# Kernel optimization log

Hardware: AMD Instinct MI355X
Metric: run time of the kernel (lower is better)

The kernel has to match this reference:

```python
import jax, jax.numpy as jnp
import numpy as np

B, C, HH, WW = 8, 512, 32, 32
HEADS, GROUPS, EPS = 8, 32, 1e-5


def setup_inputs() -> dict:
    key = jax.random.key(0)
    k0, k1, k2 = jax.random.split(key, 3)
    x = jax.random.normal(k0, (B, C, HH, WW), jnp.float32)
    gamma = jnp.ones((C,), jnp.float32)
    beta = jnp.zeros((C,), jnp.float32)
    # 1x1 convs modeled as (out, in) matrices; fan-in scaling keeps logits sane
    w_qkv = jax.random.normal(k1, (3 * C, C), jnp.float32) * (C ** -0.5)
    b_qkv = jnp.zeros((3 * C,), jnp.float32)
    w_proj = jax.random.normal(k2, (C, C), jnp.float32) * (C ** -0.5)
    b_proj = jnp.zeros((C,), jnp.float32)
    return {"x": x, "gamma": gamma, "beta": beta, "w_qkv": w_qkv,
            "b_qkv": b_qkv, "w_proj": w_proj, "b_proj": b_proj}


def reference(x, gamma, beta, w_qkv, b_qkv, w_proj, b_proj):
    b, c, h, w = x.shape
    S = h * w
    xr = x.reshape(b, c, S)
    # GroupNorm(32, C) over (channels_in_group, spatial)
    xg = xr.reshape(b, GROUPS, c // GROUPS, S)
    mu = xg.mean(axis=(2, 3), keepdims=True)
    var = xg.var(axis=(2, 3), keepdims=True)
    xn = ((xg - mu) * jax.lax.rsqrt(var + EPS)).reshape(b, c, S)
    xn = xn * gamma[None, :, None] + beta[None, :, None]
    # qkv 1x1 conv: (B, 3C, S)
    qkv = jnp.einsum('oc,bcs->bos', w_qkv, xn) + b_qkv[None, :, None]
    D = c // HEADS
    qkv = qkv.reshape(b, 3, HEADS, D, S)  # channel layout: (three, H, D)
    q = jnp.transpose(qkv[:, 0], (0, 1, 3, 2))  # (B, H, S, D)
    k = jnp.transpose(qkv[:, 1], (0, 1, 3, 2))
    v = jnp.transpose(qkv[:, 2], (0, 1, 3, 2))
    scale = 1.0 / float(np.sqrt(np.sqrt(D)))
    logits = jnp.einsum('bhtd,bhsd->bhts', q * scale, k * scale)  # (B,H,S,S)
    logits = logits - jnp.max(logits, axis=-1, keepdims=True)
    probs = jax.nn.softmax(logits, axis=-1)  # dropout p=0 (default)
    attn = jnp.einsum('bhts,bhsd->bhtd', probs, v)  # (B,H,S,D)
    hout = jnp.transpose(attn, (0, 1, 3, 2)).reshape(b, c, S)  # (B, H*D=C, S)
    hout = jnp.einsum('oc,bcs->bos', w_proj, hout) + b_proj[None, :, None]
    return (hout + xr).reshape(b, c, h, w)
```

## Files before the change

kernel.cpp:

```cpp
#include <hip/hip_runtime.h>
#include <hip/hip_bf16.h>

typedef __hip_bfloat16 bf16;
typedef unsigned short u16;
typedef __attribute__((ext_vector_type(8))) short bf16x8;
typedef __attribute__((ext_vector_type(4))) float f32x4;
typedef __attribute__((ext_vector_type(16))) float f32x16;

static constexpr int Bn = 8;
static constexpr int C = 512;
static constexpr int S = 1024;
static constexpr int NH = 8;
static constexpr int HD = 64;
static constexpr int CPG = 16;
#define EPSV 1e-5f
#define QSCALE 0.18033688011112042f

__device__ __forceinline__ u16 f2bf(float f) {
    bf16 h = __float2bfloat16(f);
    return *reinterpret_cast<u16*>(&h);
}
__device__ __forceinline__ unsigned pack_bf2(float a, float b) {
    __hip_bfloat162 h = __float22bfloat162_rn(make_float2(a, b));
    return *reinterpret_cast<unsigned*>(&h);
}

__device__ __forceinline__ void async_copy16(const void* g, void* l) {
    __builtin_amdgcn_global_load_lds(
        (const __attribute__((address_space(1))) void*)g,
        (__attribute__((address_space(3))) void*)l, 16, 0, 0);
}

__global__ __launch_bounds__(256) void prep(const float* __restrict__ x,
                                            const float* __restrict__ wqkv,
                                            const float* __restrict__ wproj,
                                            float* __restrict__ stats,
                                            u16* __restrict__ wbf) {
    const int tid = threadIdx.x;
    if (blockIdx.x < 256) {
        const int bg = blockIdx.x;
        const size_t base = (size_t)bg * CPG * S;
        const int N = CPG * S;
        float sum = 0.f, sq = 0.f;
        for (int i = tid * 4; i < N; i += 1024) {
            float4 v = *reinterpret_cast<const float4*>(&x[base + i]);
            sum += v.x + v.y + v.z + v.w;
            sq += v.x * v.x + v.y * v.y + v.z * v.z + v.w * v.w;
        }
#pragma unroll
        for (int off = 32; off > 0; off >>= 1) {
            sum += __shfl_down(sum, off, 64);
            sq  += __shfl_down(sq,  off, 64);
        }
        __shared__ float s0[4], s1[4];
        if ((tid & 63) == 0) { s0[tid >> 6] = sum; s1[tid >> 6] = sq; }
        __syncthreads();
        if (tid == 0) {
            float a  = s0[0] + s0[1] + s0[2] + s0[3];
            float b2 = s1[0] + s1[1] + s1[2] + s1[3];
            float mu = a / (float)N;
            float var = fmaxf(b2 / (float)N - mu * mu, 0.f);
            stats[bg] = mu;
            stats[256 + bg] = rsqrtf(var + EPSV);
        }
    } else {
        int idx = (blockIdx.x - 256) * 1024 + tid * 4;
        float4 v;
        float sc = 1.f;
        if (idx < 1536 * 512) {
            v = *reinterpret_cast<const float4*>(&wqkv[idx]);
            if (idx < 512 * 512) sc = QSCALE;
        } else {
            v = *reinterpret_cast<const float4*>(&wproj[idx - 1536 * 512]);
        }
        u16 t[4] = {f2bf(v.x * sc), f2bf(v.y * sc), f2bf(v.z * sc), f2bf(v.w * sc)};
        *reinterpret_cast<uint2*>(&wbf[idx]) = *reinterpret_cast<uint2*>(t);
    }
}

__global__ __launch_bounds__(256) void gn_apply_t(const float* __restrict__ x,
                                                  const float* __restrict__ gamma,
                                                  const float* __restrict__ beta,
                                                  const float* __restrict__ stats,
                                                  u16* __restrict__ xnt) {
    const int b = blockIdx.z, c0 = blockIdx.y * 64, s0 = blockIdx.x * 64;
    const int tid = threadIdx.x;
    __shared__ u16 T[64 * 72];
    const float* xb = x + ((size_t)b * C + c0) * S;
#pragma unroll
    for (int i = 0; i < 4; ++i) {
        int ch = i * 256 + tid;
        int c = ch >> 4, seg = ch & 15;
        int cg = c0 + c;
        float mu = stats[b * 32 + (cg >> 4)];
        float rstd = stats[256 + b * 32 + (cg >> 4)];
        float ga = gamma[cg], be = beta[cg];
        float4 v = *reinterpret_cast<const float4*>(&xb[(size_t)c * S + s0 + seg * 4]);
        float vals[4] = {v.x, v.y, v.z, v.w};
#pragma unroll
        for (int j = 0; j < 4; ++j)
            T[(seg * 4 + j) * 72 + c] = f2bf((vals[j] - mu) * rstd * ga + be);
    }
    __syncthreads();
#pragma unroll
    for (int i = 0; i < 2; ++i) {
        int ch = i * 256 + tid;
        int r = ch >> 3, seg = ch & 7;
        uint4 val = *reinterpret_cast<const uint4*>(&T[r * 72 + seg * 8]);
        *reinterpret_cast<uint4*>(&xnt[(size_t)(b * S + s0 + r) * C + c0 + seg * 8]) = val;
    }
}

template <int MODE>
__global__ __launch_bounds__(256) void mfma_gemm(const u16* __restrict__ Wb,
                                                 const u16* __restrict__ Xt,
                                                 const float* __restrict__ bias,
                                                 const float* __restrict__ resid,
                                                 u16* __restrict__ qkvT,
                                                 u16* __restrict__ qkvV,
                                                 float* __restrict__ Yf) {
    const int K = 512;
    const int b = blockIdx.z, o0 = blockIdx.y * 128, s0 = blockIdx.x * 128;
    const int tid = threadIdx.x;
    const int lane = tid & 63, w = tid >> 6;
    const int quad = lane >> 4, l15 = lane & 15;
    const int wr = w >> 1, wc = w & 1;
    __shared__ u16 As[128 * 64];
    __shared__ u16 Bs[128 * 64];
    f32x4 acc[4][4] = {};
    const u16* Xb = Xt + (size_t)(b * S + s0) * K;
    for (int k0 = 0; k0 < K; k0 += 64) {
#pragma unroll
        for (int i = 0; i < 4; ++i) {
            int ci = w * 4 + i;
            int r = ci * 8 + (lane >> 3);
            int c = (lane & 7) ^ (r & 7);
            async_copy16(&Wb[(size_t)(o0 + r) * K + k0 + c * 8], &As[ci * 512]);
            async_copy16(&Xb[(size_t)r * K + k0 + c * 8], &Bs[ci * 512]);
        }
        __syncthreads();
#pragma unroll
        for (int kk = 0; kk < 2; ++kk) {
            bf16x8 af[4], bfr[4];
#pragma unroll
            for (int mt = 0; mt < 4; ++mt) {
                int R = wr * 64 + mt * 16 + l15;
                af[mt] = *reinterpret_cast<const bf16x8*>(
                    &As[R * 64 + (((kk * 4 + quad) ^ (R & 7)) << 3)]);
            }
#pragma unroll
            for (int nt = 0; nt < 4; ++nt) {
                int R = wc * 64 + nt * 16 + l15;
                bfr[nt] = *reinterpret_cast<const bf16x8*>(
                    &Bs[R * 64 + (((kk * 4 + quad) ^ (R & 7)) << 3)]);
            }
#pragma unroll
            for (int mt = 0; mt < 4; ++mt)
#pragma unroll
                for (int nt = 0; nt < 4; ++nt)
                    acc[mt][nt] = __builtin_amdgcn_mfma_f32_16x16x32_bf16(
                        af[mt], bfr[nt], acc[mt][nt], 0, 0, 0);
        }
        __syncthreads();
    }
    if (MODE == 1) {
#pragma unroll
        for (int mt = 0; mt < 4; ++mt) {
#pragma unroll
            for (int reg = 0; reg < 4; ++reg) {
                int o = o0 + wr * 64 + mt * 16 + quad * 4 + reg;
                float bz = bias[o];
#pragma unroll
                for (int nt = 0; nt < 4; ++nt) {
                    int s = s0 + wc * 64 + nt * 16 + l15;
                    size_t idx = (size_t)(b * C + o) * S + s;
                    Yf[idx] = acc[mt][nt][reg] + bz + resid[idx];
                }
            }
        }
    } else if (o0 < 1024) {
        float bsc = (o0 < 512) ? QSCALE : 1.f;
#pragma unroll
        for (int mt = 0; mt < 4; ++mt) {
            int o_b = o0 + wr * 64 + mt * 16 + quad * 4;
            float bz[4];
#pragma unroll
            for (int reg = 0; reg < 4; ++reg) bz[reg] = bias[o_b + reg] * bsc;
#pragma unroll
            for (int nt = 0; nt < 4; ++nt) {
                int s = s0 + wc * 64 + nt * 16 + l15;
                uint2 pk;
                pk.x = pack_bf2(acc[mt][nt][0] + bz[0], acc[mt][nt][1] + bz[1]);
                pk.y = pack_bf2(acc[mt][nt][2] + bz[2], acc[mt][nt][3] + bz[3]);
                *reinterpret_cast<uint2*>(&qkvT[(size_t)(b * S + s) * 1024 + o_b]) = pk;
            }
        }
    } else {
#pragma unroll
        for (int mt = 0; mt < 4; ++mt) {
#pragma unroll
            for (int reg = 0; reg < 4; ++reg) {
                int o = o0 - 1024 + wr * 64 + mt * 16 + quad * 4 + reg;
                float bz = bias[o + 1024];
#pragma unroll
                for (int nt = 0; nt < 4; ++nt) {
                    int s = s0 + wc * 64 + nt * 16 + l15;
                    qkvV[(size_t)(b * 512 + o) * S + s] = f2bf(acc[mt][nt][reg] + bz);
                }
            }
        }
    }
}

__global__ __launch_bounds__(256) void attn_mfma(const u16* __restrict__ qkvT,
                                                 const u16* __restrict__ qkvV,
                                                 u16* __restrict__ houtt) {
    const int b = blockIdx.z, h = blockIdx.y, q0 = blockIdx.x * 128;
    const int tid = threadIdx.x;
    const int lane = tid & 63, w = tid >> 6;
    const int l31 = lane & 31, half = lane >> 5;
    __shared__ u16 ks[2][64 * 64];
    __shared__ u16 vs[2][64 * 64];
    __shared__ u16 ps[128 * 68];

    const u16* qrow = qkvT + (size_t)(b * S + q0 + w * 32 + l31) * 1024 + h * HD;
    const u16* krow = qkvT + (size_t)b * S * 1024 + 512 + h * HD;
    const u16* vrow = qkvV + (size_t)(b * 512 + h * HD) * S;

    bf16x8 qfrag[4];
#pragma unroll
    for (int kk = 0; kk < 4; ++kk)
        qfrag[kk] = *reinterpret_cast<const bf16x8*>(&qrow[kk * 16 + half * 8]);

#pragma unroll
    for (int i = 0; i < 2; ++i) {
        int ci = w * 2 + i;
        int r = ci * 8 + (lane >> 3);
        int c = (lane & 7) ^ (r & 7);
        async_copy16(&krow[(size_t)r * 1024 + c * 8], &ks[0][ci * 512]);
        async_copy16(&vrow[(size_t)r * S + c * 8], &vs[0][ci * 512]);
    }
    __syncthreads();

    f32x16 o_acc[2] = {};
    float l_i = 0.f;
    const int prow = (w * 32 + l31) * 68;

    for (int t = 0; t < 16; ++t) {
        const int cur = t & 1, nxt = cur ^ 1;
        if (t < 15) {
            int kt = (t + 1) * 64;
#pragma unroll
            for (int i = 0; i < 2; ++i) {
                int ci = w * 2 + i;
                int r = ci * 8 + (lane >> 3);
                int c = (lane & 7) ^ (r & 7);
                async_copy16(&krow[(size_t)(kt + r) * 1024 + c * 8], &ks[nxt][ci * 512]);
                async_copy16(&vrow[(size_t)r * S + kt + c * 8], &vs[nxt][ci * 512]);
            }
        }
        f32x16 s_acc[2] = {};
#pragma unroll
        for (int mt = 0; mt < 2; ++mt) {
            int r = mt * 32 + l31;
#pragma unroll
            for (int kk = 0; kk < 4; ++kk) {
                int c8 = kk * 2 + half;
                bf16x8 kf = *reinterpret_cast<const bf16x8*>(
                    &ks[cur][r * 64 + ((c8 ^ (r & 7)) << 3)]);
                s_acc[mt] = __builtin_amdgcn_mfma_f32_32x32x16_bf16(
                    kf, qfrag[kk], s_acc[mt], 0, 0, 0);
            }
        }
        float rs = 0.f;
#pragma unroll
        for (int mt = 0; mt < 2; ++mt)
#pragma unroll
            for (int g = 0; g < 4; ++g) {
                float p0 = __builtin_amdgcn_exp2f(s_acc[mt][g * 4 + 0]);
                float p1 = __builtin_amdgcn_exp2f(s_acc[mt][g * 4 + 1]);
                float p2 = __builtin_amdgcn_exp2f(s_acc[mt][g * 4 + 2]);
                float p3 = __builtin_amdgcn_exp2f(s_acc[mt][g * 4 + 3]);
                rs += (p0 + p1) + (p2 + p3);
                uint2 pk;
                pk.x = pack_bf2(p0, p1);
                pk.y = pack_bf2(p2, p3);
                *reinterpret_cast<uint2*>(&ps[prow + mt * 32 + g * 8 + half * 4]) = pk;
            }
        l_i += rs;
        bf16x8 pf[4];
#pragma unroll
        for (int kk = 0; kk < 4; ++kk) {
            union { uint2 u[2]; bf16x8 v; } u8;
            u8.u[0] = *reinterpret_cast<const uint2*>(&ps[prow + kk * 16 + half * 8]);
            u8.u[1] = *reinterpret_cast<const uint2*>(&ps[prow + kk * 16 + half * 8 + 4]);
            pf[kk] = u8.v;
        }
#pragma unroll
        for (int nt = 0; nt < 2; ++nt) {
            int rv = nt * 32 + l31;
#pragma unroll
            for (int kk = 0; kk < 4; ++kk) {
                int c8 = kk * 2 + half;
                bf16x8 vf = *reinterpret_cast<const bf16x8*>(
                    &vs[cur][rv * 64 + ((c8 ^ (rv & 7)) << 3)]);
                o_acc[nt] = __builtin_amdgcn_mfma_f32_32x32x16_bf16(
                    vf, pf[kk], o_acc[nt], 0, 0, 0);
            }
        }
        __syncthreads();
    }
    l_i += __shfl_xor(l_i, 32, 64);
    float inv = 1.f / l_i;
    u16* orow = houtt + (size_t)(b * S + q0 + w * 32 + l31) * 512 + h * HD;
#pragma unroll
    for (int nt = 0; nt < 2; ++nt)
#pragma unroll
        for (int g = 0; g < 4; ++g) {
            uint2 pk;
            pk.x = pack_bf2(o_acc[nt][g * 4 + 0] * inv, o_acc[nt][g * 4 + 1] * inv);
            pk.y = pack_bf2(o_acc[nt][g * 4 + 2] * inv, o_acc[nt][g * 4 + 3] * inv);
            *reinterpret_cast<uint2*>(&orow[nt * 32 + g * 8 + half * 4]) = pk;
        }
}

extern "C" void kernel_launch(void* const* d_in, const int* in_sizes, int n_in,
                              void* d_out, int out_size, void* d_ws, size_t ws_size,
                              hipStream_t stream) {
    const float* x      = (const float*)d_in[0];
    const float* gamma  = (const float*)d_in[1];
    const float* beta   = (const float*)d_in[2];
    const float* w_qkv  = (const float*)d_in[3];
    const float* b_qkv  = (const float*)d_in[4];
    const float* w_proj = (const float*)d_in[5];
    const float* b_proj = (const float*)d_in[6];
    float* out = (float*)d_out;

    char* ws = (char*)d_ws;
    float* stats = (float*)ws;
    u16* wbf   = (u16*)(ws + 4096);
    u16* xnt   = (u16*)(ws + 4096 + 2097152);
    u16* qkvT  = (u16*)(ws + 4096 + 2097152 + 8388608);
    u16* qkvV  = (u16*)(ws + 4096 + 2097152 + 8388608 + 16777216);
    u16* houtt = xnt;

    prep<<<1280, 256, 0, stream>>>(x, w_qkv, w_proj, stats, wbf);
    gn_apply_t<<<dim3(16, 8, Bn), 256, 0, stream>>>(x, gamma, beta, stats, xnt);
    mfma_gemm<0><<<dim3(8, 12, Bn), 256, 0, stream>>>(
        wbf, xnt, b_qkv, nullptr, qkvT, qkvV, nullptr);
    attn_mfma<<<dim3(8, NH, Bn), 256, 0, stream>>>(qkvT, qkvV, houtt);
    mfma_gemm<1><<<dim3(8, 4, Bn), 256, 0, stream>>>(
        wbf + 1536 * 512, houtt, b_proj, x, nullptr, nullptr, out);
}
```

Measured before the change: 160.0 us.

## Double-buffer GEMM K-loop with BK=32 and pass attention probs via lane shuffles

The projection GEMM moves from a single 64-wide K tile with two barriers per step to a double-buffered 32-wide K tile, so the async load of the next slice overlaps the MFMA work on the current one. The XOR swizzle is reworked for the 32-element row width. Separately, the attention kernel stops round-tripping the bf16 probabilities through a shared-memory scratch tile. It rebuilds the B-operand fragments in registers using cross-half __shfl_xor exchanges, which saves LDS traffic and space but adds shuffle instructions and selects.

```diff
diff --git a/kernel.cpp b/kernel.cpp
--- a/kernel.cpp
+++ b/kernel.cpp
@@ -125,42 +125,46 @@
     const int lane = tid & 63, w = tid >> 6;
     const int quad = lane >> 4, l15 = lane & 15;
     const int wr = w >> 1, wc = w & 1;
-    __shared__ u16 As[128 * 64];
-    __shared__ u16 Bs[128 * 64];
+    __shared__ u16 As[2][128 * 32];
+    __shared__ u16 Bs[2][128 * 32];
     f32x4 acc[4][4] = {};
     const u16* Xb = Xt + (size_t)(b * S + s0) * K;
-    for (int k0 = 0; k0 < K; k0 += 64) {
-#pragma unroll
-        for (int i = 0; i < 4; ++i) {
-            int ci = w * 4 + i;
-            int r = ci * 8 + (lane >> 3);
-            int c = (lane & 7) ^ (r & 7);
-            async_copy16(&Wb[(size_t)(o0 + r) * K + k0 + c * 8], &As[ci * 512]);
-            async_copy16(&Xb[(size_t)r * K + k0 + c * 8], &Bs[ci * 512]);
-        }
-        __syncthreads();
-#pragma unroll
-        for (int kk = 0; kk < 2; ++kk) {
-            bf16x8 af[4], bfr[4];
-#pragma unroll
-            for (int mt = 0; mt < 4; ++mt) {
-                int R = wr * 64 + mt * 16 + l15;
-                af[mt] = *reinterpret_cast<const bf16x8*>(
-                    &As[R * 64 + (((kk * 4 + quad) ^ (R & 7)) << 3)]);
-            }
-#pragma unroll
-            for (int nt = 0; nt < 4; ++nt) {
-                int R = wc * 64 + nt * 16 + l15;
-                bfr[nt] = *reinterpret_cast<const bf16x8*>(
-                    &Bs[R * 64 + (((kk * 4 + quad) ^ (R & 7)) << 3)]);
-            }
-#pragma unroll
-            for (int mt = 0; mt < 4; ++mt)
-#pragma unroll
-                for (int nt = 0; nt < 4; ++nt)
-                    acc[mt][nt] = __builtin_amdgcn_mfma_f32_16x16x32_bf16(
-                        af[mt], bfr[nt], acc[mt][nt], 0, 0, 0);
-        }
+    const int rA = lane >> 2, cA = lane & 3;
+
+    auto stage = [&](int bb, int k0) {
+#pragma unroll
+        for (int i = 0; i < 2; ++i) {
+            int ci = w * 2 + i;
+            int r = ci * 16 + rA;
+            int cs = cA ^ (r & 3);
+            async_copy16(&Wb[(size_t)(o0 + r) * K + k0 + cs * 8], &As[bb][ci * 512]);
+            async_copy16(&Xb[(size_t)r * K + k0 + cs * 8], &Bs[bb][ci * 512]);
+        }
+    };
+    stage(0, 0);
+    __syncthreads();
+    for (int t = 0; t < 16; ++t) {
+        const int cur = t & 1;
+        if (t < 15) stage(cur ^ 1, (t + 1) * 32);
+        bf16x8 af[4], bfr[4];
+#pragma unroll
+        for (int mt = 0; mt < 4; ++mt) {
+            int R = wr * 64 + mt * 16 + l15;
+            af[mt] = *reinterpret_cast<const bf16x8*>(
+                &As[cur][R * 32 + ((quad ^ (R & 3)) << 3)]);
+        }
+#pragma unroll
+        for (int nt = 0; nt < 4; ++nt) {
+            int R = wc * 64 + nt * 16 + l15;
+            bfr[nt] = *reinterpret_cast<const bf16x8*>(
+                &Bs[cur][R * 32 + ((quad ^ (R & 3)) << 3)]);
+        }
+#pragma unroll
+        for (int mt = 0; mt < 4; ++mt)
+#pragma unroll
+            for (int nt = 0; nt < 4; ++nt)
+                acc[mt][nt] = __builtin_amdgcn_mfma_f32_16x16x32_bf16(
+                    af[mt], bfr[nt], acc[mt][nt], 0, 0, 0);
         __syncthreads();
     }
     if (MODE == 1) {
@@ -221,7 +225,6 @@
     const int l31 = lane & 31, half = lane >> 5;
     __shared__ u16 ks[2][64 * 64];
     __shared__ u16 vs[2][64 * 64];
-    __shared__ u16 ps[128 * 68];
 
     const u16* qrow = qkvT + (size_t)(b * S + q0 + w * 32 + l31) * 1024 + h * HD;
     const u16* krow = qkvT + (size_t)b * S * 1024 + 512 + h * HD;
@@ -244,7 +247,6 @@
 
     f32x16 o_acc[2] = {};
     float l_i = 0.f;
-    const int prow = (w * 32 + l31) * 68;
 
     for (int t = 0; t < 16; ++t) {
         const int cur = t & 1, nxt = cur ^ 1;
@@ -273,6 +275,7 @@
             }
         }
         float rs = 0.f;
+        unsigned up[2][4][2];
 #pragma unroll
         for (int mt = 0; mt < 2; ++mt)
 #pragma unroll
@@ -282,20 +285,28 @@
                 float p2 = __builtin_amdgcn_exp2f(s_acc[mt][g * 4 + 2]);
                 float p3 = __builtin_amdgcn_exp2f(s_acc[mt][g * 4 + 3]);
                 rs += (p0 + p1) + (p2 + p3);
-                uint2 pk;
-                pk.x = pack_bf2(p0, p1);
-                pk.y = pack_bf2(p2, p3);
-                *reinterpret_cast<uint2*>(&ps[prow + mt * 32 + g * 8 + half * 4]) = pk;
+                up[mt][g][0] = pack_bf2(p0, p1);
+                up[mt][g][1] = pack_bf2(p2, p3);
             }
         l_i += rs;
         bf16x8 pf[4];
 #pragma unroll
-        for (int kk = 0; kk < 4; ++kk) {
-            union { uint2 u[2]; bf16x8 v; } u8;
-            u8.u[0] = *reinterpret_cast<const uint2*>(&ps[prow + kk * 16 + half * 8]);
-            u8.u[1] = *reinterpret_cast<const uint2*>(&ps[prow + kk * 16 + half * 8 + 4]);
-            pf[kk] = u8.v;
-        }
+        for (int mt = 0; mt < 2; ++mt)
+#pragma unroll
+            for (int jj = 0; jj < 2; ++jj) {
+                unsigned s0v = half ? up[mt][2 * jj][0] : up[mt][2 * jj + 1][0];
+                unsigned s1v = half ? up[mt][2 * jj][1] : up[mt][2 * jj + 1][1];
+                unsigned r0 = __shfl_xor((int)s0v, 32, 64);
+                unsigned r1 = __shfl_xor((int)s1v, 32, 64);
+                unsigned m0 = half ? up[mt][2 * jj + 1][0] : up[mt][2 * jj][0];
+                unsigned m1 = half ? up[mt][2 * jj + 1][1] : up[mt][2 * jj][1];
+                union { unsigned u4[4]; bf16x8 v; } q;
+                q.u4[0] = half ? r0 : m0;
+                q.u4[1] = half ? r1 : m1;
+                q.u4[2] = half ? m0 : r0;
+                q.u4[3] = half ? m1 : r1;
+                pf[mt * 2 + jj] = q.v;
+            }
 #pragma unroll
         for (int nt = 0; nt < 2; ++nt) {
             int rv = nt * 32 + l31;
```

New measurement: 173.2 us. +8.3%, slower.
